# Kernel tuning notes

Hardware: AMD Instinct MI355X
Metric: run time of the kernel (lower is better)

The kernel has to match this reference:

```python
import jax, jax.numpy as jnp
import numpy as np

NUM_GRAPHS = 64
NODE_SZ = 200
FEAT = 200
HID = 256          # hidden_size; each signed branch outputs HID//2
HALF = HID // 2
N_NODES = NUM_GRAPHS * NODE_SZ
N_EDGES = 409600
NUM_LAYERS = 3


def _lin_init(key, out_f, in_f):
    kw, kb = jax.random.split(key)
    s = 1.0 / np.sqrt(in_f)
    W = jax.random.uniform(kw, (out_f, in_f), minval=-s, maxval=s, dtype=jnp.float32)
    b = jax.random.uniform(kb, (out_f,), minval=-s, maxval=s, dtype=jnp.float32)
    return W, b


def setup_inputs() -> dict:
    key = jax.random.key(0)
    ks = jax.random.split(key, 16)
    x = jax.random.normal(ks[0], (N_NODES, FEAT), dtype=jnp.float32)
    edge_index = jax.random.randint(ks[1], (2, N_EDGES), 0, N_NODES, dtype=jnp.int64)
    edge_weight = jax.random.normal(ks[2], (N_EDGES,), dtype=jnp.float32)
    batch = jnp.repeat(jnp.arange(NUM_GRAPHS, dtype=jnp.int64), NODE_SZ)

    # signed conv layer params: layer0 in=FEAT, layers 1..: in=HID; each lin maps 2*in -> HALF
    Wp0, bp0 = _lin_init(ks[3], HALF, 2 * FEAT)
    Wn0, bn0 = _lin_init(ks[4], HALF, 2 * FEAT)
    Wp1, bp1 = _lin_init(ks[5], HALF, 2 * HID)
    Wn1, bn1 = _lin_init(ks[6], HALF, 2 * HID)
    Wp2, bp2 = _lin_init(ks[7], HALF, 2 * HID)
    Wn2, bn2 = _lin_init(ks[8], HALF, 2 * HID)
    Wr, br = _lin_init(ks[9], HID, NODE_SZ * HID)   # readout_lin
    Wl, bl = _lin_init(ks[10], 1, HID)              # final lin
    return dict(x=x, edge_index=edge_index, edge_weight=edge_weight, batch=batch,
                Wp0=Wp0, bp0=bp0, Wn0=Wn0, bn0=bn0,
                Wp1=Wp1, bp1=bp1, Wn1=Wn1, bn1=bn1,
                Wp2=Wp2, bp2=bp2, Wn2=Wn2, bn2=bn2,
                Wr=Wr, br=br, Wl=Wl, bl=bl)


def _signed_conv(x, src, dst, w, Wp, bp, Wn, bn):
    # edge-weighted signed mean aggregation, split by weight sign
    xs = x[src]                                   # [E, D] gather
    pw = jnp.where(w > 0, w, 0.0)
    nw = jnp.where(w < 0, -w, 0.0)
    agg_p = jax.ops.segment_sum(pw[:, None] * xs, dst, num_segments=N_NODES)
    agg_n = jax.ops.segment_sum(nw[:, None] * xs, dst, num_segments=N_NODES)
    deg_p = jax.ops.segment_sum((w > 0).astype(x.dtype), dst, num_segments=N_NODES)
    deg_n = jax.ops.segment_sum((w < 0).astype(x.dtype), dst, num_segments=N_NODES)
    agg_p = agg_p / jnp.maximum(deg_p, 1.0)[:, None]
    agg_n = agg_n / jnp.maximum(deg_n, 1.0)[:, None]
    hp = jnp.concatenate([agg_p, x], -1) @ Wp.T + bp
    hn = jnp.concatenate([agg_n, x], -1) @ Wn.T + bn
    return jnp.concatenate([hp, hn], -1)          # [N, HID]


def reference(x, edge_index, edge_weight, batch,
              Wp0, bp0, Wn0, bn0, Wp1, bp1, Wn1, bn1, Wp2, bp2, Wn2, bn2,
              Wr, br, Wl, bl):
    src, dst = edge_index[0], edge_index[1]
    convs = [(Wp0, bp0, Wn0, bn0), (Wp1, bp1, Wn1, bn1), (Wp2, bp2, Wn2, bn2)]
    h = x
    for i, (Wp, bp, Wn, bn) in enumerate(convs):
        h = _signed_conv(h, src, dst, edge_weight, Wp, bp, Wn, bn)
        if i < NUM_LAYERS - 1:
            h = jax.nn.leaky_relu(h, negative_slope=0.01)
    # per-graph readout: batch is contiguous with NODE_SZ nodes per graph,
    # so the boolean-mask+view loop is exactly a reshape.
    g = h.reshape(NUM_GRAPHS, NODE_SZ * HID)
    g = g @ Wr.T + br                             # [G, HID]
    # dropout(p=0.5) is identity in eval mode
    return g @ Wl.T + bl                          # [G, 1]
```

## Files before the change

### kernel.cpp

```cpp
#include <hip/hip_runtime.h>

#define NUM_GRAPHS 64
#define NODE_SZ    200
#define FEAT       200
#define HID        256
#define HALF       128
#define N_NODES    (NUM_GRAPHS * NODE_SZ)
#define KREAD      (NODE_SZ * HID)

typedef unsigned short ushort_t;
typedef unsigned int uint_t;
typedef __attribute__((ext_vector_type(8))) short bf16x8;
typedef __attribute__((ext_vector_type(4))) float f32x4;

#define GAS(p) ((const __attribute__((address_space(1))) void*)(p))
#define LAS(p) ((__attribute__((address_space(3))) void*)(p))

__device__ __forceinline__ float bf2f(ushort_t u) {
    union { unsigned int i; float f; } v; v.i = ((unsigned int)u) << 16; return v.f;
}
__device__ __forceinline__ ushort_t f2bf(float f) {
    union { float f; unsigned int i; } v; v.f = f;
    unsigned int x = v.i;
    unsigned int r = (x + 0x7fffu + ((x >> 16) & 1u)) >> 16;
    return (ushort_t)r;
}

__global__ __launch_bounds__(256) void prep_kernel(
        const float* __restrict__ Wp0, const float* __restrict__ Wn0,
        const float* __restrict__ Wp1, const float* __restrict__ Wn1,
        const float* __restrict__ Wp2, const float* __restrict__ Wn2,
        const float* __restrict__ x,
        uint_t* __restrict__ cntcur, ushort_t* __restrict__ wall,
        ushort_t* __restrict__ xb) {
    int gid = blockIdx.x * 256 + threadIdx.x;
    const int GS = gridDim.x * 256;
    for (int i = gid; i < 2 * N_NODES; i += GS) cntcur[i] = 0u;
    for (int idx = gid; idx < 3 * 131072; idx += GS) {
        int layer = idx >> 17, within = idx & 131071;
        int rr = within >> 8, col = within & 255;
        const float* Wp = (layer == 0) ? Wp0 : (layer == 1) ? Wp1 : Wp2;
        const float* Wn = (layer == 0) ? Wn0 : (layer == 1) ? Wn1 : Wn2;
        int Ks = (layer == 0) ? 200 : 256;
        int q = rr >> 7;
        const float* Wsrc = (q & 1) ? Wn : Wp;
        int row = rr & 127;
        int scol = col + ((q >> 1) ? Ks : 0);
        float v = (col < Ks) ? Wsrc[(size_t)row * (2 * Ks) + scol] : 0.0f;
        wall[idx] = f2bf(v);
    }
    for (int idx = gid; idx < N_NODES * 64; idx += GS) {
        int n = idx >> 6, c0 = (idx & 63) * 4;
        ushort4 o = {0, 0, 0, 0};
        if (c0 < 200) {
            float4 v = *(const float4*)&x[(size_t)n * 200 + c0];
            o.x = f2bf(v.x); o.y = f2bf(v.y); o.z = f2bf(v.z); o.w = f2bf(v.w);
        }
        *(ushort4*)&xb[(size_t)n * 256 + c0] = o;
    }
}

__global__ __launch_bounds__(512) void hist_kernel(const int* __restrict__ ei,
                                                   const float* __restrict__ ew,
                                                   uint_t* __restrict__ cnt, int E) {
    int e = blockIdx.x * 512 + threadIdx.x;
    if (e < E) {
        int dst = ei[E + e];
        float w = ew[e];
        if (w > 0.0f)      atomicAdd(&cnt[dst], 1u);
        else if (w < 0.0f) atomicAdd(&cnt[dst], 0x10000u);
    }
}

__global__ __launch_bounds__(1024) void scan_kernel(const uint_t* __restrict__ cnt,
                                                    uint2* __restrict__ obnd, int n) {
    const int PER = 13;
    int t = threadIdx.x;
    int start = t * PER;
    int local[PER];
    uint_t pcnt[PER];
    int sum = 0;
#pragma unroll
    for (int i = 0; i < PER; ++i) {
        int idx = start + i;
        uint_t c = (idx < n) ? cnt[idx] : 0u;
        int v = (int)((c & 0xffffu) + (c >> 16));
        pcnt[i] = c & 0xffffu;
        local[i] = sum;
        sum += v;
    }
    int lane = t & 63, wid = t >> 6;
    int inc = sum;
#pragma unroll
    for (int d = 1; d < 64; d <<= 1) {
        int up = __shfl_up(inc, d);
        if (lane >= d) inc += up;
    }
    __shared__ int wsum[16], woff[16];
    if (lane == 63) wsum[wid] = inc;
    __syncthreads();
    if (t < 16) {
        int acc = 0;
        for (int j = 0; j < 16; ++j) if (j < t) acc += wsum[j];
        woff[t] = acc;
    }
    __syncthreads();
    int base = woff[wid] + (inc - sum);
#pragma unroll
    for (int i = 0; i < PER; ++i) {
        int idx = start + i;
        if (idx < n) {
            uint_t off = (uint_t)(base + local[i]);
            obnd[idx] = make_uint2(off, off + pcnt[i]);
        }
    }
    if (t == 1023) {
        uint_t tot = (uint_t)(base + sum);
        obnd[n] = make_uint2(tot, tot);
    }
}

__device__ __forceinline__ void gemm_body(int t, const ushort_t* __restrict__ A,
                                          const ushort_t* __restrict__ Bw,
                                          ushort_t* __restrict__ Y,
                                          ushort_t* smem) {
    int mBase = (t >> 1) * 128;
    int nBase = (t & 1) * 256;
    int tid  = threadIdx.x;
    int lane = tid & 63;
    int wv   = tid >> 6;
    int r    = lane & 15;
    int quad = lane >> 4;
    int wm   = wv >> 1;
    int wn   = wv & 1;

    int rowA = tid >> 2, colc = (tid & 3) * 8;
    const ushort_t* gA  = A  + (size_t)(mBase + rowA) * 256 + colc;
    const ushort_t* gB0 = Bw + (size_t)(nBase + rowA) * 256 + colc;
    const ushort_t* gB1 = Bw + (size_t)(nBase + 128 + rowA) * 256 + colc;

    f32x4 acc[2][8];
#pragma unroll
    for (int i = 0; i < 2; ++i)
#pragma unroll
        for (int j = 0; j < 8; ++j) acc[i][j] = (f32x4){0.f, 0.f, 0.f, 0.f};

    auto STAGE = [&](int buf, int kb) {
        ushort_t* Ad = smem + (buf << 12) + tid * 8;
        ushort_t* Bd = smem + 8192 + (buf << 13) + tid * 8;
        __builtin_amdgcn_global_load_lds(GAS(gA + kb), LAS(Ad), 16, 0, 0);
        __builtin_amdgcn_global_load_lds(GAS(gB0 + kb), LAS(Bd), 16, 0, 0);
        __builtin_amdgcn_global_load_lds(GAS(gB1 + kb), LAS(Bd + 4096), 16, 0, 0);
    };

    STAGE(0, 0);
    for (int kt = 0; kt < 8; ++kt) {
        int cb = kt & 1;
        __syncthreads();
        if (kt < 7) STAGE(cb ^ 1, (kt + 1) * 32);
        const ushort_t* Ac = smem + (cb << 12);
        const ushort_t* Bc = smem + 8192 + (cb << 13);
        bf16x8 af[2];
#pragma unroll
        for (int i = 0; i < 2; ++i)
            af[i] = *(const bf16x8*)&Ac[(wm * 32 + i * 16 + r) * 32 + quad * 8];
#pragma unroll
        for (int j = 0; j < 8; ++j) {
            bf16x8 bfr = *(const bf16x8*)&Bc[(wn * 128 + j * 16 + r) * 32 + quad * 8];
            acc[0][j] = __builtin_amdgcn_mfma_f32_16x16x32_bf16(af[0], bfr, acc[0][j], 0, 0, 0);
            acc[1][j] = __builtin_amdgcn_mfma_f32_16x16x32_bf16(af[1], bfr, acc[1][j], 0, 0, 0);
        }
    }
#pragma unroll
    for (int i = 0; i < 2; ++i)
#pragma unroll
        for (int j = 0; j < 8; ++j) {
            int c = nBase + wn * 128 + j * 16 + r;
#pragma unroll
            for (int reg = 0; reg < 4; ++reg) {
                int m = mBase + wm * 32 + i * 16 + quad * 4 + reg;
                Y[(size_t)m * 512 + c] = f2bf(acc[i][j][reg]);
            }
        }
}

__global__ __launch_bounds__(512) void scatgemm_kernel(
        const int* __restrict__ ei, const float* __restrict__ ew,
        const uint2* __restrict__ obnd, uint_t* __restrict__ cur,
        uint2* __restrict__ es, int E,
        const ushort_t* __restrict__ xb, const ushort_t* __restrict__ wall,
        ushort_t* __restrict__ Yall) {
    __shared__ __align__(16) ushort_t smem[24576];
    int bx = blockIdx.x;
    if (bx < 200) {
        gemm_body(bx, xb, wall, Yall, smem);
        return;
    }
    int e = (bx - 200) * 512 + threadIdx.x;
    if (e < E) {
        int src = ei[e];
        int dst = ei[E + e];
        float w = ew[e];
        if (w > 0.0f) {
            uint_t old = atomicAdd(&cur[dst], 1u);
            es[obnd[dst].x + (old & 0xffffu)] = make_uint2((uint_t)src, __float_as_uint(w));
        } else if (w < 0.0f) {
            uint_t old = atomicAdd(&cur[dst], 0x10000u);
            es[obnd[dst].y + (old >> 16)] = make_uint2((uint_t)src, __float_as_uint(-w));
        }
    }
}

__global__ __launch_bounds__(512) void gemm_kernel(const ushort_t* __restrict__ A,
                                                   const ushort_t* __restrict__ Bw,
                                                   ushort_t* __restrict__ Y) {
    __shared__ __align__(16) ushort_t smem[24576];
    gemm_body(blockIdx.x, A, Bw, Y, smem);
}

template <bool LEAKY>
__global__ __launch_bounds__(256) void agg_kernel(
        const ushort_t* __restrict__ Y,
        const uint2* __restrict__ obnd,
        const uint2* __restrict__ es,
        const float* __restrict__ bp, const float* __restrict__ bn,
        ushort_t* __restrict__ outp) {
    int lane = threadIdx.x & 63;
    int wv   = threadIdx.x >> 6;
    int n = blockIdx.x * 4 + wv;
    int c0 = lane * 2;
    uint2 ob = obnd[n];
    uint_t off = ob.x, mid = ob.y, end = obnd[n + 1].x;

    float accp[2] = {0.f, 0.f};
    float accn[2] = {0.f, 0.f};

#pragma unroll 1
    for (int phase = 0; phase < 2; ++phase) {
        uint_t lo = phase ? mid : off;
        uint_t hi = phase ? end : mid;
        float* acc = phase ? accn : accp;
        const ushort_t* Yb = Y + (phase ? 128 : 0) + c0;
#pragma unroll 1
        for (uint_t base = lo; base < hi; base += 64) {
            int cnt = (int)min(64u, hi - base);
            uint2 rec = es[base + (uint_t)min(lane, cnt - 1)];
            int i = 0;
#pragma unroll 1
            for (; i + 8 <= cnt; i += 8) {
                int s[8]; float w[8]; uint_t u[8];
#pragma unroll
                for (int j = 0; j < 8; ++j) {
                    s[j] = __shfl((int)rec.x, i + j);
                    w[j] = __uint_as_float((uint_t)__shfl((int)rec.y, i + j));
                }
#pragma unroll
                for (int j = 0; j < 8; ++j) u[j] = *(const uint_t*)&Yb[(size_t)s[j] * 512];
#pragma unroll
                for (int j = 0; j < 8; ++j) {
                    acc[0] = fmaf(w[j], bf2f((ushort_t)(u[j] & 0xffffu)), acc[0]);
                    acc[1] = fmaf(w[j], bf2f((ushort_t)(u[j] >> 16)), acc[1]);
                }
            }
#pragma unroll 1
            for (; i < cnt; ++i) {
                int s = __shfl((int)rec.x, i);
                float w = __uint_as_float((uint_t)__shfl((int)rec.y, i));
                uint_t u = *(const uint_t*)&Yb[(size_t)s * 512];
                acc[0] = fmaf(w, bf2f((ushort_t)(u & 0xffffu)), acc[0]);
                acc[1] = fmaf(w, bf2f((ushort_t)(u >> 16)), acc[1]);
            }
        }
    }

    float dp = fmaxf((float)(mid - off), 1.0f);
    float dn = fmaxf((float)(end - mid), 1.0f);
    float rp = 1.0f / dp, rn = 1.0f / dn;
    uint_t zp = *(const uint_t*)&Y[(size_t)n * 512 + 256 + c0];
    uint_t zn = *(const uint_t*)&Y[(size_t)n * 512 + 384 + c0];
    float vp0 = fmaf(accp[0], rp, bf2f((ushort_t)(zp & 0xffffu)) + bp[c0]);
    float vp1 = fmaf(accp[1], rp, bf2f((ushort_t)(zp >> 16))     + bp[c0 + 1]);
    float vn0 = fmaf(accn[0], rn, bf2f((ushort_t)(zn & 0xffffu)) + bn[c0]);
    float vn1 = fmaf(accn[1], rn, bf2f((ushort_t)(zn >> 16))     + bn[c0 + 1]);
    if (LEAKY) {
        vp0 = (vp0 > 0.0f) ? vp0 : 0.01f * vp0;
        vp1 = (vp1 > 0.0f) ? vp1 : 0.01f * vp1;
        vn0 = (vn0 > 0.0f) ? vn0 : 0.01f * vn0;
        vn1 = (vn1 > 0.0f) ? vn1 : 0.01f * vn1;
    }
    uint_t op = (uint_t)f2bf(vp0) | ((uint_t)f2bf(vp1) << 16);
    uint_t on = (uint_t)f2bf(vn0) | ((uint_t)f2bf(vn1) << 16);
    *(uint_t*)&outp[(size_t)n * 256 + c0]       = op;
    *(uint_t*)&outp[(size_t)n * 256 + 128 + c0] = on;
}

__global__ __launch_bounds__(256) void readout_mfma(
        const ushort_t* __restrict__ h, const float* __restrict__ Wr,
        float* __restrict__ partial) {
    __shared__ __align__(16) ushort_t As[64 * 32];
    __shared__ __align__(16) ushort_t Bs[64 * 32];
    int nBase  = blockIdx.x * 64;
    int kStart = blockIdx.y * 800;
    int tid  = threadIdx.x;
    int lane = tid & 63;
    int wv   = tid >> 6;
    int r    = lane & 15;
    int quad = lane >> 4;

    f32x4 acc[4];
#pragma unroll
    for (int j = 0; j < 4; ++j) acc[j] = (f32x4){0.f, 0.f, 0.f, 0.f};

    for (int kt = 0; kt < 25; ++kt) {
        int kBase = kStart + kt * 32;
        int lin = tid * 8;
        int row = lin >> 5, col = lin & 31;
        *(uint4*)&As[lin] = *(const uint4*)&h[(size_t)row * KREAD + kBase + col];
        {
            const float* wp = &Wr[(size_t)(nBase + row) * KREAD + kBase + col];
            float4 f0 = *(const float4*)&wp[0];
            float4 f1 = *(const float4*)&wp[4];
            ushort4 b0, b1;
            b0.x = f2bf(f0.x); b0.y = f2bf(f0.y); b0.z = f2bf(f0.z); b0.w = f2bf(f0.w);
            b1.x = f2bf(f1.x); b1.y = f2bf(f1.y); b1.z = f2bf(f1.z); b1.w = f2bf(f1.w);
            *(ushort4*)&Bs[lin]     = b0;
            *(ushort4*)&Bs[lin + 4] = b1;
        }
        __syncthreads();
        bf16x8 a = *(const bf16x8*)&As[(wv * 16 + r) * 32 + quad * 8];
#pragma unroll
        for (int j = 0; j < 4; ++j) {
            bf16x8 b = *(const bf16x8*)&Bs[(j * 16 + r) * 32 + quad * 8];
            acc[j] = __builtin_amdgcn_mfma_f32_16x16x32_bf16(a, b, acc[j], 0, 0, 0);
        }
        __syncthreads();
    }
    float* out = partial + (size_t)blockIdx.y * (64 * HID);
#pragma unroll
    for (int j = 0; j < 4; ++j) {
        int c = nBase + j * 16 + r;
#pragma unroll
        for (int reg = 0; reg < 4; ++reg) {
            int g = wv * 16 + quad * 4 + reg;
            out[g * HID + c] = acc[j][reg];
        }
    }
}

__global__ void final_kernel(const float* __restrict__ partial, const float* __restrict__ br,
                             const float* __restrict__ Wl, const float* __restrict__ bl,
                             float* __restrict__ out) {
    int g = blockIdx.x;
    int c = threadIdx.x;
    float s = 0.0f;
#pragma unroll 4
    for (int k = 0; k < 64; ++k) s += partial[(size_t)k * (64 * HID) + g * HID + c];
    float v = (s + br[c]) * Wl[c];
#pragma unroll
    for (int d = 32; d > 0; d >>= 1) v += __shfl_down(v, d);
    __shared__ float sh[4];
    if ((c & 63) == 0) sh[c >> 6] = v;
    __syncthreads();
    if (c == 0) out[g] = sh[0] + sh[1] + sh[2] + sh[3] + bl[0];
}

extern "C" void kernel_launch(void* const* d_in, const int* in_sizes, int n_in,
                              void* d_out, int out_size, void* d_ws, size_t ws_size,
                              hipStream_t stream) {
    const float* x  = (const float*)d_in[0];
    const int*   ei = (const int*)d_in[1];
    const float* ew = (const float*)d_in[2];
    const float* Wp0 = (const float*)d_in[4];
    const float* bp0 = (const float*)d_in[5];
    const float* Wn0 = (const float*)d_in[6];
    const float* bn0 = (const float*)d_in[7];
    const float* Wp1 = (const float*)d_in[8];
    const float* bp1 = (const float*)d_in[9];
    const float* Wn1 = (const float*)d_in[10];
    const float* bn1 = (const float*)d_in[11];
    const float* Wp2 = (const float*)d_in[12];
    const float* bp2 = (const float*)d_in[13];
    const float* Wn2 = (const float*)d_in[14];
    const float* bn2 = (const float*)d_in[15];
    const float* Wr  = (const float*)d_in[16];
    const float* br  = (const float*)d_in[17];
    const float* Wl  = (const float*)d_in[18];
    const float* bl  = (const float*)d_in[19];
    const int E = in_sizes[1] / 2;

    char* ws = (char*)d_ws;
    float*    partial = (float*)(ws);
    uint_t*   cnt     = (uint_t*)(ws + 4194304);
    uint_t*   cur     = (uint_t*)(ws + 4245504);
    uint2*    obnd    = (uint2*)(ws + 4296704);
    uint2*    es      = (uint2*)(ws + 4399168);
    ushort_t* Yall    = (ushort_t*)(ws + 7675968);
    ushort_t* hA      = (ushort_t*)(ws + 20783168);
    ushort_t* hB      = (ushort_t*)(ws + 27336768);
    ushort_t* wall    = (ushort_t*)(ws + 33890368);
    ushort_t* xb      = (ushort_t*)(ws + 34676800);

    hipLaunchKernelGGL(prep_kernel, dim3(512), dim3(256), 0, stream,
                       Wp0, Wn0, Wp1, Wn1, Wp2, Wn2, x, cnt, wall, xb);
    hipLaunchKernelGGL(hist_kernel, dim3((E + 511) / 512), dim3(512), 0, stream, ei, ew, cnt, E);
    hipLaunchKernelGGL(scan_kernel, dim3(1), dim3(1024), 0, stream, cnt, obnd, N_NODES);
    hipLaunchKernelGGL(scatgemm_kernel, dim3(200 + (E + 511) / 512), dim3(512), 0, stream,
                       ei, ew, obnd, cur, es, E, xb, wall, Yall);
    hipLaunchKernelGGL((agg_kernel<true>), dim3(N_NODES / 4), dim3(256), 0, stream,
                       Yall, obnd, es, bp0, bn0, hA);
    hipLaunchKernelGGL(gemm_kernel, dim3(200), dim3(512), 0, stream, hA, wall + 131072, Yall);
    hipLaunchKernelGGL((agg_kernel<true>), dim3(N_NODES / 4), dim3(256), 0, stream,
                       Yall, obnd, es, bp1, bn1, hB);
    hipLaunchKernelGGL(gemm_kernel, dim3(200), dim3(512), 0, stream, hB, wall + 262144, Yall);
    hipLaunchKernelGGL((agg_kernel<false>), dim3(N_NODES / 4), dim3(256), 0, stream,
                       Yall, obnd, es, bp2, bn2, hA);
    hipLaunchKernelGGL(readout_mfma, dim3(4, 64), dim3(256), 0, stream, hA, Wr, partial);
    hipLaunchKernelGGL(final_kernel, dim3(NUM_GRAPHS), dim3(256), 0, stream,
                       partial, br, Wl, bl, (float*)d_out);
}
```

Before: 303.7 us.

## Fold readout into precomputed Wl·Wr vector and merge hist/scan/prep into one kernel

The two readout linears are collapsed algebraically into a single weight vector weff = Wl·Wr, computed in fp32 alongside prep. The final aggregation dots each node's output with weff and atomically adds into the per-graph output, which removes the readout GEMM, the partial buffer and the final kernel. Prep, histogram and scan are merged into one launch, with the scan run by the last block to finish. The histogram atomics now record per-edge ranks, so the scatter pass needs no second round of atomics. Float atomics make the summation order nondeterministic, and the fused launch depends on a last-block-done counter that must be zeroed before each call.

```diff
diff --git a/kernel.cpp b/kernel.cpp
--- a/kernel.cpp
+++ b/kernel.cpp
@@ -26,97 +26,132 @@
     return (ushort_t)r;
 }
 
-__global__ __launch_bounds__(256) void prep_kernel(
+#define OFF_CNT    0
+#define OFF_DONE   51200
+#define OFF_WEFF   51264
+#define OFF_OBND   256064
+#define OFF_RANK   358472
+#define OFF_ES     1177672
+#define OFF_YALL   4454480
+#define OFF_HA     17561680
+#define OFF_HB     24115280
+#define OFF_WALL   30668880
+#define OFF_XB     31455312
+
+__global__ __launch_bounds__(1024) void k1_kernel(
         const float* __restrict__ Wp0, const float* __restrict__ Wn0,
         const float* __restrict__ Wp1, const float* __restrict__ Wn1,
         const float* __restrict__ Wp2, const float* __restrict__ Wn2,
-        const float* __restrict__ x,
-        uint_t* __restrict__ cntcur, ushort_t* __restrict__ wall,
-        ushort_t* __restrict__ xb) {
-    int gid = blockIdx.x * 256 + threadIdx.x;
-    const int GS = gridDim.x * 256;
-    for (int i = gid; i < 2 * N_NODES; i += GS) cntcur[i] = 0u;
-    for (int idx = gid; idx < 3 * 131072; idx += GS) {
-        int layer = idx >> 17, within = idx & 131071;
-        int rr = within >> 8, col = within & 255;
-        const float* Wp = (layer == 0) ? Wp0 : (layer == 1) ? Wp1 : Wp2;
-        const float* Wn = (layer == 0) ? Wn0 : (layer == 1) ? Wn1 : Wn2;
-        int Ks = (layer == 0) ? 200 : 256;
-        int q = rr >> 7;
-        const float* Wsrc = (q & 1) ? Wn : Wp;
-        int row = rr & 127;
-        int scol = col + ((q >> 1) ? Ks : 0);
-        float v = (col < Ks) ? Wsrc[(size_t)row * (2 * Ks) + scol] : 0.0f;
-        wall[idx] = f2bf(v);
-    }
-    for (int idx = gid; idx < N_NODES * 64; idx += GS) {
-        int n = idx >> 6, c0 = (idx & 63) * 4;
-        ushort4 o = {0, 0, 0, 0};
-        if (c0 < 200) {
-            float4 v = *(const float4*)&x[(size_t)n * 200 + c0];
-            o.x = f2bf(v.x); o.y = f2bf(v.y); o.z = f2bf(v.z); o.w = f2bf(v.w);
-        }
-        *(ushort4*)&xb[(size_t)n * 256 + c0] = o;
-    }
-}
-
-__global__ __launch_bounds__(512) void hist_kernel(const int* __restrict__ ei,
-                                                   const float* __restrict__ ew,
-                                                   uint_t* __restrict__ cnt, int E) {
-    int e = blockIdx.x * 512 + threadIdx.x;
-    if (e < E) {
-        int dst = ei[E + e];
-        float w = ew[e];
-        if (w > 0.0f)      atomicAdd(&cnt[dst], 1u);
-        else if (w < 0.0f) atomicAdd(&cnt[dst], 0x10000u);
-    }
-}
-
-__global__ __launch_bounds__(1024) void scan_kernel(const uint_t* __restrict__ cnt,
-                                                    uint2* __restrict__ obnd, int n) {
-    const int PER = 13;
-    int t = threadIdx.x;
-    int start = t * PER;
-    int local[PER];
-    uint_t pcnt[PER];
-    int sum = 0;
-#pragma unroll
-    for (int i = 0; i < PER; ++i) {
-        int idx = start + i;
-        uint_t c = (idx < n) ? cnt[idx] : 0u;
-        int v = (int)((c & 0xffffu) + (c >> 16));
-        pcnt[i] = c & 0xffffu;
-        local[i] = sum;
-        sum += v;
-    }
-    int lane = t & 63, wid = t >> 6;
-    int inc = sum;
-#pragma unroll
-    for (int d = 1; d < 64; d <<= 1) {
-        int up = __shfl_up(inc, d);
-        if (lane >= d) inc += up;
-    }
-    __shared__ int wsum[16], woff[16];
-    if (lane == 63) wsum[wid] = inc;
+        const float* __restrict__ x, const float* __restrict__ Wr,
+        const float* __restrict__ Wl,
+        const int* __restrict__ ei, const float* __restrict__ ew, int E,
+        uint_t* __restrict__ cnt, ushort_t* __restrict__ rank16,
+        ushort_t* __restrict__ wall, ushort_t* __restrict__ xb,
+        float* __restrict__ weff, uint_t* __restrict__ done,
+        uint2* __restrict__ obnd, int nblk) {
+    int bx = blockIdx.x, tid = threadIdx.x;
+    if (bx < 50) {
+        for (int idx = bx * 1024 + tid; idx < N_NODES * 64; idx += 51200) {
+            int n = idx >> 6, c0 = (idx & 63) * 4;
+            ushort4 o = {0, 0, 0, 0};
+            if (c0 < 200) {
+                float4 v = *(const float4*)&x[(size_t)n * 200 + c0];
+                o.x = f2bf(v.x); o.y = f2bf(v.y); o.z = f2bf(v.z); o.w = f2bf(v.w);
+            }
+            *(ushort4*)&xb[(size_t)n * 256 + c0] = o;
+        }
+    } else if (bx < 98) {
+        for (int idx = (bx - 50) * 1024 + tid; idx < 3 * 131072; idx += 49152) {
+            int layer = idx >> 17, within = idx & 131071;
+            int rr = within >> 8, col = within & 255;
+            const float* Wp = (layer == 0) ? Wp0 : (layer == 1) ? Wp1 : Wp2;
+            const float* Wn = (layer == 0) ? Wn0 : (layer == 1) ? Wn1 : Wn2;
+            int Ks = (layer == 0) ? 200 : 256;
+            int q = rr >> 7;
+            const float* Wsrc = (q & 1) ? Wn : Wp;
+            int row = rr & 127;
+            int scol = col + ((q >> 1) ? Ks : 0);
+            float v = (col < Ks) ? Wsrc[(size_t)row * (2 * Ks) + scol] : 0.0f;
+            wall[idx] = f2bf(v);
+        }
+    } else if (bx < 148) {
+        int k = (bx - 98) * 1024 + tid;
+        float s0 = 0.f, s1 = 0.f, s2 = 0.f, s3 = 0.f;
+#pragma unroll 1
+        for (int c = 0; c < 256; c += 4) {
+            s0 = fmaf(Wl[c + 0], Wr[(size_t)(c + 0) * KREAD + k], s0);
+            s1 = fmaf(Wl[c + 1], Wr[(size_t)(c + 1) * KREAD + k], s1);
+            s2 = fmaf(Wl[c + 2], Wr[(size_t)(c + 2) * KREAD + k], s2);
+            s3 = fmaf(Wl[c + 3], Wr[(size_t)(c + 3) * KREAD + k], s3);
+        }
+        weff[k] = (s0 + s1) + (s2 + s3);
+    } else {
+        int e = (bx - 148) * 1024 + tid;
+        if (e < E) {
+            int dst = ei[E + e];
+            float w = ew[e];
+            if (w > 0.0f) {
+                uint_t old = atomicAdd(&cnt[dst], 1u);
+                rank16[e] = (ushort_t)(old & 0xffffu);
+            } else if (w < 0.0f) {
+                uint_t old = atomicAdd(&cnt[dst], 0x10000u);
+                rank16[e] = (ushort_t)(old >> 16);
+            }
+        }
+    }
+
     __syncthreads();
-    if (t < 16) {
-        int acc = 0;
-        for (int j = 0; j < 16; ++j) if (j < t) acc += wsum[j];
-        woff[t] = acc;
-    }
+    __threadfence();
+    __shared__ uint_t lastFlag;
+    if (tid == 0)
+        lastFlag = (atomicAdd(done, 1u) == (uint_t)(nblk - 1)) ? 1u : 0u;
     __syncthreads();
-    int base = woff[wid] + (inc - sum);
-#pragma unroll
-    for (int i = 0; i < PER; ++i) {
-        int idx = start + i;
-        if (idx < n) {
-            uint_t off = (uint_t)(base + local[i]);
-            obnd[idx] = make_uint2(off, off + pcnt[i]);
-        }
-    }
-    if (t == 1023) {
-        uint_t tot = (uint_t)(base + sum);
-        obnd[n] = make_uint2(tot, tot);
+    if (lastFlag) {
+        __threadfence();
+        const int PER = 13;
+        int t = tid;
+        int start = t * PER;
+        int local[PER];
+        uint_t pcnt[PER];
+        int sum = 0;
+#pragma unroll
+        for (int i = 0; i < PER; ++i) {
+            int idx = start + i;
+            uint_t c = (idx < N_NODES) ? cnt[idx] : 0u;
+            int v = (int)((c & 0xffffu) + (c >> 16));
+            pcnt[i] = c & 0xffffu;
+            local[i] = sum;
+            sum += v;
+        }
+        int lane = t & 63, wid = t >> 6;
+        int inc = sum;
+#pragma unroll
+        for (int d = 1; d < 64; d <<= 1) {
+            int up = __shfl_up(inc, d);
+            if (lane >= d) inc += up;
+        }
+        __shared__ int wsum[16], woff[16];
+        if (lane == 63) wsum[wid] = inc;
+        __syncthreads();
+        if (t < 16) {
+            int acc = 0;
+            for (int j = 0; j < 16; ++j) if (j < t) acc += wsum[j];
+            woff[t] = acc;
+        }
+        __syncthreads();
+        int base = woff[wid] + (inc - sum);
+#pragma unroll
+        for (int i = 0; i < PER; ++i) {
+            int idx = start + i;
+            if (idx < N_NODES) {
+                uint_t off = (uint_t)(base + local[i]);
+                obnd[idx] = make_uint2(off, off + pcnt[i]);
+            }
+        }
+        if (t == 1023) {
+            uint_t tot = (uint_t)(base + sum);
+            obnd[N_NODES] = make_uint2(tot, tot);
+        }
     }
 }
 
@@ -186,7 +221,7 @@
 
 __global__ __launch_bounds__(512) void scatgemm_kernel(
         const int* __restrict__ ei, const float* __restrict__ ew,
-        const uint2* __restrict__ obnd, uint_t* __restrict__ cur,
+        const uint2* __restrict__ obnd, const ushort_t* __restrict__ rank16,
         uint2* __restrict__ es, int E,
         const ushort_t* __restrict__ xb, const ushort_t* __restrict__ wall,
         ushort_t* __restrict__ Yall) {
@@ -201,13 +236,11 @@
         int src = ei[e];
         int dst = ei[E + e];
         float w = ew[e];
-        if (w > 0.0f) {
-            uint_t old = atomicAdd(&cur[dst], 1u);
-            es[obnd[dst].x + (old & 0xffffu)] = make_uint2((uint_t)src, __float_as_uint(w));
-        } else if (w < 0.0f) {
-            uint_t old = atomicAdd(&cur[dst], 0x10000u);
-            es[obnd[dst].y + (old >> 16)] = make_uint2((uint_t)src, __float_as_uint(-w));
-        }
+        uint_t rk = rank16[e];
+        if (w > 0.0f)
+            es[obnd[dst].x + rk] = make_uint2((uint_t)src, __float_as_uint(w));
+        else if (w < 0.0f)
+            es[obnd[dst].y + rk] = make_uint2((uint_t)src, __float_as_uint(-w));
     }
 }
 
@@ -218,17 +251,30 @@
     gemm_body(blockIdx.x, A, Bw, Y, smem);
 }
 
-template <bool LEAKY>
+template <bool LEAKY, bool DOT>
 __global__ __launch_bounds__(256) void agg_kernel(
         const ushort_t* __restrict__ Y,
         const uint2* __restrict__ obnd,
         const uint2* __restrict__ es,
         const float* __restrict__ bp, const float* __restrict__ bn,
-        ushort_t* __restrict__ outp) {
+        ushort_t* __restrict__ outp,
+        const float* __restrict__ weff,
+        float* __restrict__ outg,
+        const float* __restrict__ br, const float* __restrict__ Wl,
+        const float* __restrict__ bl) {
     int lane = threadIdx.x & 63;
     int wv   = threadIdx.x >> 6;
     int n = blockIdx.x * 4 + wv;
     int c0 = lane * 2;
+
+    if (DOT && blockIdx.x < NUM_GRAPHS && wv == 0) {
+        float p = br[lane] * Wl[lane] + br[lane + 64] * Wl[lane + 64]
+                + br[lane + 128] * Wl[lane + 128] + br[lane + 192] * Wl[lane + 192];
+#pragma unroll
+        for (int d = 32; d > 0; d >>= 1) p += __shfl_xor(p, d);
+        if (lane == 0) atomicAdd(&outg[blockIdx.x], p + bl[0]);
+    }
+
     uint2 ob = obnd[n];
     uint_t off = ob.x, mid = ob.y, end = obnd[n + 1].x;
 
@@ -288,80 +334,20 @@
         vn0 = (vn0 > 0.0f) ? vn0 : 0.01f * vn0;
         vn1 = (vn1 > 0.0f) ? vn1 : 0.01f * vn1;
     }
-    uint_t op = (uint_t)f2bf(vp0) | ((uint_t)f2bf(vp1) << 16);
-    uint_t on = (uint_t)f2bf(vn0) | ((uint_t)f2bf(vn1) << 16);
-    *(uint_t*)&outp[(size_t)n * 256 + c0]       = op;
-    *(uint_t*)&outp[(size_t)n * 256 + 128 + c0] = on;
-}
-
-__global__ __launch_bounds__(256) void readout_mfma(
-        const ushort_t* __restrict__ h, const float* __restrict__ Wr,
-        float* __restrict__ partial) {
-    __shared__ __align__(16) ushort_t As[64 * 32];
-    __shared__ __align__(16) ushort_t Bs[64 * 32];
-    int nBase  = blockIdx.x * 64;
-    int kStart = blockIdx.y * 800;
-    int tid  = threadIdx.x;
-    int lane = tid & 63;
-    int wv   = tid >> 6;
-    int r    = lane & 15;
-    int quad = lane >> 4;
-
-    f32x4 acc[4];
-#pragma unroll
-    for (int j = 0; j < 4; ++j) acc[j] = (f32x4){0.f, 0.f, 0.f, 0.f};
-
-    for (int kt = 0; kt < 25; ++kt) {
-        int kBase = kStart + kt * 32;
-        int lin = tid * 8;
-        int row = lin >> 5, col = lin & 31;
-        *(uint4*)&As[lin] = *(const uint4*)&h[(size_t)row * KREAD + kBase + col];
-        {
-            const float* wp = &Wr[(size_t)(nBase + row) * KREAD + kBase + col];
-            float4 f0 = *(const float4*)&wp[0];
-            float4 f1 = *(const float4*)&wp[4];
-            ushort4 b0, b1;
-            b0.x = f2bf(f0.x); b0.y = f2bf(f0.y); b0.z = f2bf(f0.z); b0.w = f2bf(f0.w);
-            b1.x = f2bf(f1.x); b1.y = f2bf(f1.y); b1.z = f2bf(f1.z); b1.w = f2bf(f1.w);
-            *(ushort4*)&Bs[lin]     = b0;
-            *(ushort4*)&Bs[lin + 4] = b1;
-        }
-        __syncthreads();
-        bf16x8 a = *(const bf16x8*)&As[(wv * 16 + r) * 32 + quad * 8];
-#pragma unroll
-        for (int j = 0; j < 4; ++j) {
-            bf16x8 b = *(const bf16x8*)&Bs[(j * 16 + r) * 32 + quad * 8];
-            acc[j] = __builtin_amdgcn_mfma_f32_16x16x32_bf16(a, b, acc[j], 0, 0, 0);
-        }
-        __syncthreads();
-    }
-    float* out = partial + (size_t)blockIdx.y * (64 * HID);
-#pragma unroll
-    for (int j = 0; j < 4; ++j) {
-        int c = nBase + j * 16 + r;
-#pragma unroll
-        for (int reg = 0; reg < 4; ++reg) {
-            int g = wv * 16 + quad * 4 + reg;
-            out[g * HID + c] = acc[j][reg];
-        }
-    }
-}
-
-__global__ void final_kernel(const float* __restrict__ partial, const float* __restrict__ br,
-                             const float* __restrict__ Wl, const float* __restrict__ bl,
-                             float* __restrict__ out) {
-    int g = blockIdx.x;
-    int c = threadIdx.x;
-    float s = 0.0f;
-#pragma unroll 4
-    for (int k = 0; k < 64; ++k) s += partial[(size_t)k * (64 * HID) + g * HID + c];
-    float v = (s + br[c]) * Wl[c];
-#pragma unroll
-    for (int d = 32; d > 0; d >>= 1) v += __shfl_down(v, d);
-    __shared__ float sh[4];
-    if ((c & 63) == 0) sh[c >> 6] = v;
-    __syncthreads();
-    if (c == 0) out[g] = sh[0] + sh[1] + sh[2] + sh[3] + bl[0];
+    if (DOT) {
+        int g = n / 200;
+        int kbase = (n - g * 200) * 256;
+        float s = vp0 * weff[kbase + c0] + vp1 * weff[kbase + c0 + 1]
+                + vn0 * weff[kbase + 128 + c0] + vn1 * weff[kbase + 128 + c0 + 1];
+#pragma unroll
+        for (int d = 32; d > 0; d >>= 1) s += __shfl_xor(s, d);
+        if (lane == 0) atomicAdd(&outg[g], s);
+    } else {
+        uint_t op = (uint_t)f2bf(vp0) | ((uint_t)f2bf(vp1) << 16);
+        uint_t on = (uint_t)f2bf(vn0) | ((uint_t)f2bf(vn1) << 16);
+        *(uint_t*)&outp[(size_t)n * 256 + c0]       = op;
+        *(uint_t*)&outp[(size_t)n * 256 + 128 + c0] = on;
+    }
 }
 
 extern "C" void kernel_launch(void* const* d_in, const int* in_sizes, int n_in,
@@ -389,32 +375,40 @@
     const int E = in_sizes[1] / 2;
 
     char* ws = (char*)d_ws;
-    float*    partial = (float*)(ws);
-    uint_t*   cnt     = (uint_t*)(ws + 4194304);
-    uint_t*   cur     = (uint_t*)(ws + 4245504);
-    uint2*    obnd    = (uint2*)(ws + 4296704);
-    uint2*    es      = (uint2*)(ws + 4399168);
-    ushort_t* Yall    = (ushort_t*)(ws + 7675968);
-    ushort_t* hA      = (ushort_t*)(ws + 20783168);
-    ushort_t* hB      = (ushort_t*)(ws + 27336768);
-    ushort_t* wall    = (ushort_t*)(ws + 33890368);
-    ushort_t* xb      = (ushort_t*)(ws + 34676800);
-
-    hipLaunchKernelGGL(prep_kernel, dim3(512), dim3(256), 0, stream,
-                       Wp0, Wn0, Wp1, Wn1, Wp2, Wn2, x, cnt, wall, xb);
-    hipLaunchKernelGGL(hist_kernel, dim3((E + 511) / 512), dim3(512), 0, stream, ei, ew, cnt, E);
-    hipLaunchKernelGGL(scan_kernel, dim3(1), dim3(1024), 0, stream, cnt, obnd, N_NODES);
+    uint_t*   cnt    = (uint_t*)(ws + OFF_CNT);
+    uint_t*   done   = (uint_t*)(ws + OFF_DONE);
+    float*    weff   = (float*)(ws + OFF_WEFF);
+    uint2*    obnd   = (uint2*)(ws + OFF_OBND);
+    ushort_t* rank16 = (ushort_t*)(ws + OFF_RANK);
+    uint2*    es     = (uint2*)(ws + OFF_ES);
+    ushort_t* Yall   = (ushort_t*)(ws + OFF_YALL);
+    ushort_t* hA     = (ushort_t*)(ws + OFF_HA);
+    ushort_t* hB     = (ushort_t*)(ws + OFF_HB);
+    ushort_t* wall   = (ushort_t*)(ws + OFF_WALL);
+    ushort_t* xb     = (ushort_t*)(ws + OFF_XB);
+    float*    outg   = (float*)d_out;
+
+    hipMemsetAsync(ws + OFF_CNT, 0, 51200 + 64, stream);
+    hipMemsetAsync(d_out, 0, out_size, stream);
+
+    int histBlocks = (E + 1023) / 1024;
+    int k1Grid = 148 + histBlocks;
+    hipLaunchKernelGGL(k1_kernel, dim3(k1Grid), dim3(1024), 0, stream,
+                       Wp0, Wn0, Wp1, Wn1, Wp2, Wn2, x, Wr, Wl,
+                       ei, ew, E, cnt, rank16, wall, xb, weff, done, obnd, k1Grid);
     hipLaunchKernelGGL(scatgemm_kernel, dim3(200 + (E + 511) / 512), dim3(512), 0, stream,
-                       ei, ew, obnd, cur, es, E, xb, wall, Yall);
-    hipLaunchKernelGGL((agg_kernel<true>), dim3(N_NODES / 4), dim3(256), 0, stream,
-                       Yall, obnd, es, bp0, bn0, hA);
+                       ei, ew, obnd, rank16, es, E, xb, wall, Yall);
+    hipLaunchKernelGGL((agg_kernel<true, false>), dim3(N_NODES / 4), dim3(256), 0, stream,
+                       Yall, obnd, es, bp0, bn0, hA, (const float*)nullptr,
+                       (float*)nullptr, (const float*)nullptr, (const float*)nullptr,
+                       (const float*)nullptr);
     hipLaunchKernelGGL(gemm_kernel, dim3(200), dim3(512), 0, stream, hA, wall + 131072, Yall);
-    hipLaunchKernelGGL((agg_kernel<true>), dim3(N_NODES / 4), dim3(256), 0, stream,
-                       Yall, obnd, es, bp1, bn1, hB);
+    hipLaunchKernelGGL((agg_kernel<true, false>), dim3(N_NODES / 4), dim3(256), 0, stream,
+                       Yall, obnd, es, bp1, bn1, hB, (const float*)nullptr,
+                       (float*)nullptr, (const float*)nullptr, (const float*)nullptr,
+                       (const float*)nullptr);
     hipLaunchKernelGGL(gemm_kernel, dim3(200), dim3(512), 0, stream, hB, wall + 262144, Yall);
-    hipLaunchKernelGGL((agg_kernel<false>), dim3(N_NODES / 4), dim3(256), 0, stream,
-                       Yall, obnd, es, bp2, bn2, hA);
-    hipLaunchKernelGGL(readout_mfma, dim3(4, 64), dim3(256), 0, stream, hA, Wr, partial);
-    hipLaunchKernelGGL(final_kernel, dim3(NUM_GRAPHS), dim3(256), 0, stream,
-                       partial, br, Wl, bl, (float*)d_out);
-}
+    hipLaunchKernelGGL((agg_kernel<false, true>), dim3(N_NODES / 4), dim3(256), 0, stream,
+                       Yall, obnd, es, bp2, bn2, (ushort_t*)nullptr, weff,
+                       outg, br, Wl, bl);
+}
```

New measurement: 584.9 us. +92.6%, slower.
